# Performance work log

Hardware: AMD Instinct MI355X
Metric: run time of the kernel (lower is better)

## Reference

```python
import jax, jax.numpy as jnp
import numpy as np

EPS = 1e-8


def setup_inputs() -> dict:
    key = jax.random.key(0)
    k1, k2, k3, k4 = jax.random.split(key, 4)
    batch, n_obs, hist = 64, 2048, 512
    values = jax.random.normal(k1, (batch, n_obs, hist), dtype=jnp.float32)
    means = jax.random.normal(k2, (n_obs,), dtype=jnp.float32)
    counts = jax.random.randint(k3, (n_obs,), 0, 1000, dtype=jnp.int32)
    # M2 = var * count, keep it positive and roughly scaled with count
    M2s = jax.random.uniform(k4, (n_obs,), dtype=jnp.float32) * counts.astype(jnp.float32)
    sig_ids = jnp.arange(n_obs, dtype=jnp.int32)  # one unique signature per obs column
    return {"values": values, "means": means, "M2s": M2s, "counts": counts, "sig_ids": sig_ids}


def reference(values, means, M2s, counts, sig_ids):
    """Training-mode forward: Welford merge of running per-signature stats with the
    batch of last-timestep values, then normalize full history with merged stats.

    values: [b, n, h] float; means/M2s: [n_sigs]; counts: [n_sigs] int; sig_ids: [n] int.
    """
    b = values.shape[0]
    v = values[:, :, -1]                      # [b, n] last timestep per obs
    mean_new = jnp.mean(v, axis=0)            # [n]
    var_new = jnp.var(v, axis=0)              # biased (ddof=0), matches unbiased=False
    count_new = jnp.float32(b)
    M2_new = var_new * count_new              # [n]

    # gather prior stats per observation column
    c = counts[sig_ids].astype(jnp.float32)   # [n]
    m = means[sig_ids]                        # [n]
    M2 = M2s[sig_ids]                         # [n]

    # Welford parallel merge (matches update())
    delta = mean_new - m
    total = c + count_new
    m_merged = m + delta * (count_new / total)
    M2_merged = M2 + M2_new + delta * delta * c * count_new / total

    # stats are stored detached (torch.no_grad + .detach())
    m_merged = jax.lax.stop_gradient(m_merged)
    M2_merged = jax.lax.stop_gradient(M2_merged)
    total = jax.lax.stop_gradient(total)

    var = M2_merged / total
    std = jnp.sqrt(var + EPS)                 # [n]
    normed = (values - m_merged[None, :, None]) / std[None, :, None]
    # count < 2 -> passthrough (matches normalize())
    ok = (total >= 2.0)[None, :, None]
    return jnp.where(ok, normed, values)
```

## Files before the change

kernel.cpp:

```cpp
#include <hip/hip_runtime.h>
#include <math.h>

#define EPS 1e-8f

__global__ void sig_stats_kernel(const float* __restrict__ values,
                                 const float* __restrict__ means,
                                 const float* __restrict__ M2s,
                                 const int* __restrict__ counts,
                                 const int* __restrict__ sig_ids,
                                 float2* __restrict__ ss,
                                 int n_obs, int hist, int batch) {
    int wave = (int)((blockIdx.x * blockDim.x + threadIdx.x) >> 6);
    int lane = (int)(threadIdx.x & 63);
    if (wave >= n_obs) return;

    float v = 0.0f;
    if (lane < batch) {
        long long idx = (long long)lane * n_obs * hist + (long long)wave * hist + (hist - 1);
        v = values[idx];
    }

    float s = v;
    #pragma unroll
    for (int o = 32; o > 0; o >>= 1) s += __shfl_xor(s, o, 64);
    float cnt_new = (float)batch;
    float mean_new = s / cnt_new;

    float d = (lane < batch) ? (v - mean_new) : 0.0f;
    float sq = d * d;
    #pragma unroll
    for (int o = 32; o > 0; o >>= 1) sq += __shfl_xor(sq, o, 64);
    float M2_new = sq;

    if (lane == 0) {
        int id = sig_ids[wave];
        float c  = (float)counts[id];
        float m  = means[id];
        float M2 = M2s[id];
        float delta = mean_new - m;
        float total = c + cnt_new;
        float m_merged  = m + delta * (cnt_new / total);
        float M2_merged = M2 + M2_new + delta * delta * c * cnt_new / total;
        float var = M2_merged / total;
        float stdv = sqrtf(var + EPS);
        bool ok = (total >= 2.0f);
        float sc = ok ? (1.0f / stdv) : 1.0f;
        float sh = ok ? (-m_merged / stdv) : 0.0f;
        ss[wave] = make_float2(sc, sh);
    }
}

__global__ __launch_bounds__(256) void sig_norm_kernel(const float4* __restrict__ vals,
                                                       const float2* __restrict__ ss,
                                                       float4* __restrict__ out,
                                                       int n_obs, int h4, int rows) {
    int gwave  = (int)((blockIdx.x * blockDim.x + threadIdx.x) >> 6);
    int lane   = (int)(threadIdx.x & 63);
    int nwaves = (int)((gridDim.x * blockDim.x) >> 6);

    for (int row = gwave; row < rows; row += nwaves) {
        int n = row % n_obs;
        float2 st = ss[n];
        long long base = (long long)row * h4;
        #pragma unroll 2
        for (int j = lane; j < h4; j += 64) {
            float4 v = vals[base + j];
            float4 o;
            o.x = fmaf(v.x, st.x, st.y);
            o.y = fmaf(v.y, st.x, st.y);
            o.z = fmaf(v.z, st.x, st.y);
            o.w = fmaf(v.w, st.x, st.y);
            out[base + j] = o;
        }
    }
}

extern "C" void kernel_launch(void* const* d_in, const int* in_sizes, int n_in,
                              void* d_out, int out_size, void* d_ws, size_t ws_size,
                              hipStream_t stream) {
    const float* values  = (const float*)d_in[0];
    const float* means   = (const float*)d_in[1];
    const float* M2s     = (const float*)d_in[2];
    const int*   counts  = (const int*)d_in[3];
    const int*   sig_ids = (const int*)d_in[4];
    float* out = (float*)d_out;

    const int batch = 64;
    int n_obs = in_sizes[1];
    long long total = (long long)in_sizes[0];
    int hist = (int)(total / ((long long)batch * n_obs));

    float2* ss = (float2*)d_ws;

    int waves_per_block = 4;
    int blocks1 = (n_obs + waves_per_block - 1) / waves_per_block;
    sig_stats_kernel<<<blocks1, 256, 0, stream>>>(values, means, M2s, counts, sig_ids,
                                                  ss, n_obs, hist, batch);

    int h4 = hist / 4;
    int rows = batch * n_obs;
    int blocks2 = 2048;
    sig_norm_kernel<<<blocks2, 256, 0, stream>>>((const float4*)values, ss,
                                                 (float4*)out, n_obs, h4, rows);
}
```

Before: 444.5 us.

## Fuse per-column stats and normalization into one kernel with recomputed stats

Merges the stats kernel and the normalization kernel into one launch. Each wave takes an (obs column, group of 16 batch rows) work item, recomputes that column's batch mean/variance and the Welford merge itself, then normalizes the 16 rows. This drops a kernel launch and the workspace round-trip, but each column's strided gather of last-timestep values is now repeated for every group, and the inner loop is no longer unrolled.

```diff
diff --git a/kernel.cpp b/kernel.cpp
--- a/kernel.cpp
+++ b/kernel.cpp
@@ -3,74 +3,72 @@
 
 #define EPS 1e-8f
 
-__global__ void sig_stats_kernel(const float* __restrict__ values,
-                                 const float* __restrict__ means,
-                                 const float* __restrict__ M2s,
-                                 const int* __restrict__ counts,
-                                 const int* __restrict__ sig_ids,
-                                 float2* __restrict__ ss,
-                                 int n_obs, int hist, int batch) {
-    int wave = (int)((blockIdx.x * blockDim.x + threadIdx.x) >> 6);
-    int lane = (int)(threadIdx.x & 63);
-    if (wave >= n_obs) return;
+typedef float __attribute__((ext_vector_type(4))) f32x4;
 
-    float v = 0.0f;
-    if (lane < batch) {
-        long long idx = (long long)lane * n_obs * hist + (long long)wave * hist + (hist - 1);
-        v = values[idx];
-    }
+__global__ __launch_bounds__(256) void sig_fused_kernel(
+    const float* __restrict__ values,
+    const float* __restrict__ means,
+    const float* __restrict__ M2s,
+    const int* __restrict__ counts,
+    const int* __restrict__ sig_ids,
+    float* __restrict__ out,
+    int n_obs, int hist, int batch, int rpw, int total_work) {
 
-    float s = v;
-    #pragma unroll
-    for (int o = 32; o > 0; o >>= 1) s += __shfl_xor(s, o, 64);
-    float cnt_new = (float)batch;
-    float mean_new = s / cnt_new;
+    int gwave  = (int)((blockIdx.x * blockDim.x + threadIdx.x) >> 6);
+    int lane   = (int)(threadIdx.x & 63);
+    int nwaves = (int)((gridDim.x * blockDim.x) >> 6);
+    int h4 = hist >> 2;
+    const f32x4* vals4 = (const f32x4*)values;
+    f32x4* out4 = (f32x4*)out;
 
-    float d = (lane < batch) ? (v - mean_new) : 0.0f;
-    float sq = d * d;
-    #pragma unroll
-    for (int o = 32; o > 0; o >>= 1) sq += __shfl_xor(sq, o, 64);
-    float M2_new = sq;
+    for (int w = gwave; w < total_work; w += nwaves) {
+        int n  = w % n_obs;
+        int bg = w / n_obs;
 
-    if (lane == 0) {
-        int id = sig_ids[wave];
+        float v = 0.0f;
+        if (lane < batch) {
+            long long idx = ((long long)lane * n_obs + n) * hist + (hist - 1);
+            v = values[idx];
+        }
+        float s = v;
+        #pragma unroll
+        for (int o = 32; o > 0; o >>= 1) s += __shfl_xor(s, o, 64);
+        float cnt_new = (float)batch;
+        float mean_new = s / cnt_new;
+
+        float d = (lane < batch) ? (v - mean_new) : 0.0f;
+        float sq = d * d;
+        #pragma unroll
+        for (int o = 32; o > 0; o >>= 1) sq += __shfl_xor(sq, o, 64);
+        float M2_new = sq;
+
+        int id = sig_ids[n];
         float c  = (float)counts[id];
         float m  = means[id];
         float M2 = M2s[id];
         float delta = mean_new - m;
-        float total = c + cnt_new;
-        float m_merged  = m + delta * (cnt_new / total);
-        float M2_merged = M2 + M2_new + delta * delta * c * cnt_new / total;
-        float var = M2_merged / total;
+        float totalc = c + cnt_new;
+        float m_merged  = m + delta * (cnt_new / totalc);
+        float M2_merged = M2 + M2_new + delta * delta * c * cnt_new / totalc;
+        float var = M2_merged / totalc;
         float stdv = sqrtf(var + EPS);
-        bool ok = (total >= 2.0f);
+        bool ok = (totalc >= 2.0f);
         float sc = ok ? (1.0f / stdv) : 1.0f;
         float sh = ok ? (-m_merged / stdv) : 0.0f;
-        ss[wave] = make_float2(sc, sh);
-    }
-}
 
-__global__ __launch_bounds__(256) void sig_norm_kernel(const float4* __restrict__ vals,
-                                                       const float2* __restrict__ ss,
-                                                       float4* __restrict__ out,
-                                                       int n_obs, int h4, int rows) {
-    int gwave  = (int)((blockIdx.x * blockDim.x + threadIdx.x) >> 6);
-    int lane   = (int)(threadIdx.x & 63);
-    int nwaves = (int)((gridDim.x * blockDim.x) >> 6);
-
-    for (int row = gwave; row < rows; row += nwaves) {
-        int n = row % n_obs;
-        float2 st = ss[n];
-        long long base = (long long)row * h4;
-        #pragma unroll 2
-        for (int j = lane; j < h4; j += 64) {
-            float4 v = vals[base + j];
-            float4 o;
-            o.x = fmaf(v.x, st.x, st.y);
-            o.y = fmaf(v.y, st.x, st.y);
-            o.z = fmaf(v.z, st.x, st.y);
-            o.w = fmaf(v.w, st.x, st.y);
-            out[base + j] = o;
+        int b0   = bg * rpw;
+        int bend = b0 + rpw; if (bend > batch) bend = batch;
+        for (int b = b0; b < bend; ++b) {
+            long long base = ((long long)b * n_obs + n) * h4;
+            for (int j = lane; j < h4; j += 64) {
+                f32x4 x = vals4[base + j];
+                f32x4 o;
+                o.x = fmaf(x.x, sc, sh);
+                o.y = fmaf(x.y, sc, sh);
+                o.z = fmaf(x.z, sc, sh);
+                o.w = fmaf(x.w, sc, sh);
+                out4[base + j] = o;
+            }
         }
     }
 }
@@ -90,16 +88,12 @@
     long long total = (long long)in_sizes[0];
     int hist = (int)(total / ((long long)batch * n_obs));
 
-    float2* ss = (float2*)d_ws;
+    const int rpw = 16;
+    int groups = (batch + rpw - 1) / rpw;
+    int total_work = n_obs * groups;
 
-    int waves_per_block = 4;
-    int blocks1 = (n_obs + waves_per_block - 1) / waves_per_block;
-    sig_stats_kernel<<<blocks1, 256, 0, stream>>>(values, means, M2s, counts, sig_ids,
-                                                  ss, n_obs, hist, batch);
-
-    int h4 = hist / 4;
-    int rows = batch * n_obs;
-    int blocks2 = 2048;
-    sig_norm_kernel<<<blocks2, 256, 0, stream>>>((const float4*)values, ss,
-                                                 (float4*)out, n_obs, h4, rows);
+    int blocks = (total_work + 3) / 4;
+    if (blocks > 2048) blocks = 2048;
+    sig_fused_kernel<<<blocks, 256, 0, stream>>>(values, means, M2s, counts, sig_ids,
+                                                 out, n_obs, hist, batch, rpw, total_work);
 }
```

After: 454.6 us. 2.3% more time.
